# Kernel optimization log

Measured on AMD Instinct MI355X. Metric: run time of the kernel, lower is better.

Reference implementation:

```python
import jax, jax.numpy as jnp
import numpy as np
import math

B, S, D = 4, 4096, 1024
H, DH = 16, 64          # n_heads x head_dim = d_model
INTER = 4096            # intermediate_size
CAP = int(S * 0.25)     # MoD capacity = capacity_factor * seq_len = 1024


def rmsnorm(x, w, eps=1e-6):
    return x * jax.lax.rsqrt(jnp.mean(x * x, axis=-1, keepdims=True) + eps) * w


def setup_inputs() -> dict:
    key = jax.random.key(0)
    ks = jax.random.split(key, 12)
    s = 1.0 / math.sqrt(D)
    return {
        "hidden_states": jax.random.normal(ks[0], (B, S, D), jnp.float32),
        "ssm_norm_w": jnp.ones((D,), jnp.float32),
        "ssm_a": jax.random.normal(ks[1], (D,), jnp.float32),
        "ssm_gain": jax.random.normal(ks[2], (D,), jnp.float32) * 0.1,
        "router_w": jax.random.normal(ks[3], (D,), jnp.float32) * s,
        "attn_norm_w": jnp.ones((D,), jnp.float32),
        "wq": jax.random.normal(ks[4], (D, D), jnp.float32) * s,
        "wk": jax.random.normal(ks[5], (D, D), jnp.float32) * s,
        "wv": jax.random.normal(ks[6], (D, D), jnp.float32) * s,
        "wo": jax.random.normal(ks[7], (D, D), jnp.float32) * s,
        "ffn_norm_w": jnp.ones((D,), jnp.float32),
        "w1": jax.random.normal(ks[8], (D, INTER), jnp.float32) * s,
        "w2": jax.random.normal(ks[9], (INTER, D), jnp.float32) / math.sqrt(INTER),
    }


def reference(hidden_states, ssm_norm_w, ssm_a, ssm_gain, router_w, attn_norm_w,
              wq, wk, wv, wo, ffn_norm_w, w1, w2):
    # --- SSM layer (pre-norm diagonal linear recurrence + residual) ---
    xb = rmsnorm(hidden_states, ssm_norm_w)
    decay = jax.nn.sigmoid(ssm_a)  # [D] per-channel state decay

    def step(hprev, xt):  # xt: [B, D]
        hnew = decay * hprev + (1.0 - decay) * xt
        return hnew, hnew

    _, ys = jax.lax.scan(step, jnp.zeros((B, D), jnp.float32), jnp.swapaxes(xb, 0, 1))
    h = hidden_states + jnp.swapaxes(ys, 0, 1) * ssm_gain  # [B, S, D]

    # --- MoD router: pick top-CAP tokens per sequence ---
    scores = jnp.einsum('bsd,d->bs', h, router_w)            # [B, S]
    _, idx = jax.lax.top_k(scores, CAP)                      # [B, C]
    idx = jnp.sort(idx, axis=-1)                             # keep causal order
    weights = jax.nn.sigmoid(jnp.take_along_axis(scores, idx, axis=1))  # [B, C]
    aux_loss = jnp.mean(jax.nn.sigmoid(scores))              # router load aux

    # --- gather selected tokens -> attention ---
    sel = jnp.take_along_axis(h, idx[:, :, None], axis=1)    # [B, C, D]
    xn = rmsnorm(sel, attn_norm_w)
    q = (xn @ wq).reshape(B, CAP, H, DH)
    k = (xn @ wk).reshape(B, CAP, H, DH)
    v = (xn @ wv).reshape(B, CAP, H, DH)
    att = jnp.einsum('bqhd,bkhd->bhqk', q, k) / math.sqrt(DH)
    causal = jnp.tril(jnp.ones((CAP, CAP), bool))
    att = jnp.where(causal, att, jnp.float32(-1e30))
    p = jax.nn.softmax(att, axis=-1)
    o = jnp.einsum('bhqk,bkhd->bqhd', p, v).reshape(B, CAP, D)
    attn_out = o @ wo                                        # [B, C, D]

    # --- weighted scatter_add back onto the residual stream ---
    b_idx = jnp.arange(B)[:, None]
    h = h.at[b_idx, idx].add(attn_out * weights[:, :, None])

    # --- dense FFN residual (non-MoE layer) ---
    xf = rmsnorm(h, ffn_norm_w)
    h = h + jax.nn.silu(xf @ w1) @ w2
    return h, aux_loss
```

## Files before the change

kernel.cpp:

```cpp
#include <hip/hip_runtime.h>

typedef unsigned short u16;
typedef unsigned int   u32;
typedef __attribute__((ext_vector_type(4))) float f32x4;
typedef __attribute__((ext_vector_type(8))) __bf16 bf16x8;
typedef __attribute__((ext_vector_type(8))) unsigned short u16x8;

#define DEV __device__ __forceinline__

DEV u16 f2bf(float f){
  u32 u = __builtin_bit_cast(u32, f);
  u32 r = (u + 0x7fffu + ((u >> 16) & 1u)) >> 16;
  return (u16)r;
}

DEV f32x4 mfma16(bf16x8 a, bf16x8 b, f32x4 c){
  return __builtin_amdgcn_mfma_f32_16x16x32_bf16(a, b, c, 0, 0, 0);
}

DEV void gload16(const void* g, void* l){
  __builtin_amdgcn_global_load_lds((const __attribute__((address_space(1))) u32*)g,
                                   (__attribute__((address_space(3))) u32*)l, 16, 0, 0);
}

DEV int swz16(int r, int g){ return r*64 + 8*(g ^ (r&7) ^ ((r>>3)&7)); }
DEV int swze (int r, int e){ return r*64 + (e&7) + 8*(((e>>3) ^ (r&7) ^ ((r>>3)&7))); }

__global__ __launch_bounds__(256) void transpose_cast(const float* __restrict__ src,
                                                      u16* __restrict__ dst, int R, int C){
  __shared__ float tile[32][33];
  int r  = threadIdx.x >> 3;
  int c4 = (threadIdx.x & 7) * 4;
  int r0 = blockIdx.x * 32, c0 = blockIdx.y * 32;
  float4 v = *(const float4*)&src[(size_t)(r0 + r) * C + c0 + c4];
  tile[r][c4+0] = v.x; tile[r][c4+1] = v.y; tile[r][c4+2] = v.z; tile[r][c4+3] = v.w;
  __syncthreads();
  ushort4 o;
  o.x = f2bf(tile[c4+0][r]);
  o.y = f2bf(tile[c4+1][r]);
  o.z = f2bf(tile[c4+2][r]);
  o.w = f2bf(tile[c4+3][r]);
  *(ushort4*)&dst[(size_t)(c0 + r) * R + r0 + c4] = o;
}

__global__ __launch_bounds__(256) void rms_inv_k(const float* __restrict__ x, float* __restrict__ inv){
  int row  = blockIdx.x * 4 + (threadIdx.x >> 6);
  int lane = threadIdx.x & 63;
  const float* p = x + (size_t)row * 1024;
  float ss = 0.f;
  #pragma unroll
  for (int j = 0; j < 4; ++j){
    float4 v = *(const float4*)&p[lane*4 + j*256];
    ss += v.x*v.x + v.y*v.y + v.z*v.z + v.w*v.w;
  }
  #pragma unroll
  for (int o = 1; o < 64; o <<= 1) ss += __shfl_xor(ss, o);
  if (lane == 0) inv[row] = 1.f / sqrtf(ss * (1.f/1024.f) + 1e-6f);
}

__global__ __launch_bounds__(1024) void ssm_a_k(const float* __restrict__ hid, const float* __restrict__ invr,
    const float* __restrict__ nw, const float* __restrict__ av, float* __restrict__ Fc){
  int c = blockIdx.x & 63, b = blockIdx.x >> 6;
  int d = threadIdx.x;
  float w   = nw[d];
  float dec = 1.f/(1.f + expf(-av[d]));
  float od  = 1.f - dec;
  const float* hp = hid + ((size_t)b*4096 + c*64)*1024 + d;
  const float* ip = invr + b*4096 + c*64;
  float hs = 0.f;
  for (int i = 0; i < 64; ++i)
    hs = dec*hs + od*(hp[(size_t)i*1024] * ip[i] * w);
  Fc[((size_t)b*64 + c)*1024 + d] = hs;
}
__global__ __launch_bounds__(1024) void ssm_b_k(const float* __restrict__ Fc, float* __restrict__ Init,
                                                const float* __restrict__ av){
  int b  = blockIdx.x >> 6;
  int dg = blockIdx.x & 63;
  int dl = threadIdx.x >> 6;
  int c  = threadIdx.x & 63;
  int d  = dg*16 + dl;
  float dec = 1.f/(1.f + expf(-av[d]));
  float a = powf(dec, 64.f);
  float x = Fc[((size_t)(b*64 + c))*1024 + d];
  float coef = a;
  #pragma unroll
  for (int s = 1; s < 64; s <<= 1){
    float prev = __shfl_up(x, s, 64);
    if (c >= s) x += coef * prev;
    coef *= coef;
  }
  float ex = __shfl_up(x, 1, 64);
  Init[((size_t)(b*64 + c))*1024 + d] = (c > 0) ? ex : 0.f;
}
__global__ __launch_bounds__(1024) void ssm_c_k(const float* __restrict__ hid, const float* __restrict__ invr,
    const float* __restrict__ nw, const float* __restrict__ av, const float* __restrict__ gn,
    const float* __restrict__ Init, float* __restrict__ hout){
  int c = blockIdx.x & 63, b = blockIdx.x >> 6;
  int d = threadIdx.x;
  float w   = nw[d];
  float g   = gn[d];
  float dec = 1.f/(1.f + expf(-av[d]));
  float od  = 1.f - dec;
  size_t rowoff = ((size_t)b*4096 + c*64)*1024 + d;
  const float* hp = hid + rowoff;
  float* op = hout + rowoff;
  const float* ip = invr + b*4096 + c*64;
  float hs = Init[((size_t)b*64 + c)*1024 + d];
  for (int i = 0; i < 64; ++i){
    float hv = hp[(size_t)i*1024];
    hs = dec*hs + od*(hv * ip[i] * w);
    op[(size_t)i*1024] = hv + hs*g;
  }
}

__global__ __launch_bounds__(256) void score_k(const float* __restrict__ h, const float* __restrict__ rw,
                                               float* __restrict__ sc){
  int row  = blockIdx.x * 4 + (threadIdx.x >> 6);
  int lane = threadIdx.x & 63;
  const float* p = h + (size_t)row * 1024;
  float s = 0.f;
  #pragma unroll
  for (int j = 0; j < 4; ++j){
    float4 v = *(const float4*)&p[lane*4 + j*256];
    float4 w = *(const float4*)&rw[lane*4 + j*256];
    s += v.x*w.x + v.y*w.y + v.z*w.z + v.w*w.w;
  }
  #pragma unroll
  for (int o = 1; o < 64; o <<= 1) s += __shfl_xor(s, o);
  if (lane == 0) sc[row] = s;
}

__global__ __launch_bounds__(256) void aux_k(const float* __restrict__ sc, float* __restrict__ out){
  __shared__ float red[256];
  int tid = threadIdx.x;
  float s = 0.f;
  for (int i = tid; i < 16384; i += 256) s += 1.f/(1.f + expf(-sc[i]));
  red[tid] = s; __syncthreads();
  for (int o = 128; o > 0; o >>= 1){ if (tid < o) red[tid] += red[tid+o]; __syncthreads(); }
  if (tid == 0) out[0] = red[0] * (1.f/16384.f);
}

__global__ __launch_bounds__(1024) void topk_k(const float* __restrict__ sc, int* __restrict__ idx,
                                               float* __restrict__ wsel){
  __shared__ float sv[4096];
  __shared__ int   si[4096];
  int b = blockIdx.x, tid = threadIdx.x;
  for (int i = tid; i < 4096; i += 1024){ sv[i] = sc[b*4096 + i]; si[i] = i; }
  __syncthreads();
  for (int k = 2; k <= 4096; k <<= 1)
    for (int j = k >> 1; j > 0; j >>= 1){
      for (int i = tid; i < 4096; i += 1024){
        int p = i ^ j;
        if (p > i){
          float vi = sv[i], vp = sv[p];
          int ii = si[i], ip = si[p];
          bool before = (vi > vp) || (vi == vp && ii < ip);
          bool desc = ((i & k) == 0);
          if (desc ? !before : before){ sv[i]=vp; sv[p]=vi; si[i]=ip; si[p]=ii; }
        }
      }
      __syncthreads();
    }
  for (int k = 2; k <= 1024; k <<= 1)
    for (int j = k >> 1; j > 0; j >>= 1){
      int i = tid, p = i ^ j;
      if (p > i){
        int a = si[i], c = si[p];
        bool asc = ((i & k) == 0);
        if (asc ? (a > c) : (a < c)){ si[i] = c; si[p] = a; }
      }
      __syncthreads();
    }
  int t = si[tid];
  idx[b*1024 + tid]  = t;
  wsel[b*1024 + tid] = 1.f/(1.f + expf(-sc[b*4096 + t]));
}

__global__ __launch_bounds__(256) void rownorm_bf16_k(const float* __restrict__ src, const float* __restrict__ w,
    u16* __restrict__ dst, const int* __restrict__ gidx, int base){
  int row  = blockIdx.x * 4 + (threadIdx.x >> 6);
  int lane = threadIdx.x & 63;
  size_t srow;
  if (gidx){ int b = row >> 10; srow = (size_t)b*4096 + gidx[row]; }
  else srow = (size_t)(base + row);
  const float* p = src + srow*1024;
  float4 v[4]; float ss = 0.f;
  #pragma unroll
  for (int j = 0; j < 4; ++j){
    v[j] = *(const float4*)&p[lane*4 + j*256];
    ss += v[j].x*v[j].x + v[j].y*v[j].y + v[j].z*v[j].z + v[j].w*v[j].w;
  }
  #pragma unroll
  for (int o = 1; o < 64; o <<= 1) ss += __shfl_xor(ss, o);
  float inv = 1.f / sqrtf(ss * (1.f/1024.f) + 1e-6f);
  #pragma unroll
  for (int j = 0; j < 4; ++j){
    float4 wv = *(const float4*)&w[lane*4 + j*256];
    ushort4 o4;
    o4.x = f2bf(v[j].x*inv*wv.x);
    o4.y = f2bf(v[j].y*inv*wv.y);
    o4.z = f2bf(v[j].z*inv*wv.z);
    o4.w = f2bf(v[j].w*inv*wv.w);
    *(ushort4*)&dst[(size_t)row*1024 + lane*4 + j*256] = o4;
  }
}

template<int BM, int BN, int EPI>
__global__ __launch_bounds__(256) void gemmk(const u16* __restrict__ A, const u16* __restrict__ BT,
    u16* __restrict__ Cb, float* __restrict__ Cf, int M, int N, int K,
    const int* __restrict__ gidx, const float* __restrict__ wsel){
  constexpr int WROWS = BM / 2;
  constexpr int WCOLS = BN / 2;
  constexpr int MI = WROWS / 16;
  constexpr int NI = WCOLS / 16;
  constexpr int AR = BM / 32;
  constexpr int BR = BN / 32;
  __shared__ u16 As[2][BM*64];
  __shared__ u16 Bs[2][BN*64];

  int tid = threadIdx.x, wave = tid >> 6, lane = tid & 63;
  int lr = lane & 15, lg = lane >> 4;
  int wm = wave >> 1, wn = wave & 1;

  int lin = blockIdx.x + gridDim.x * blockIdx.y;
  int nwg = gridDim.x * gridDim.y;
  int q8 = nwg >> 3, r8 = nwg & 7;
  int xc = lin & 7, of = lin >> 3;
  int sw = (xc < r8 ? xc*(q8+1) : r8*(q8+1) + (xc-r8)*q8) + of;
  int bm = sw % gridDim.x, bn = sw / gridDim.x;

  f32x4 zero4 = {0.f,0.f,0.f,0.f};
  f32x4 acc[MI][NI];
  #pragma unroll
  for (int mi = 0; mi < MI; ++mi)
    #pragma unroll
    for (int ni = 0; ni < NI; ++ni) acc[mi][ni] = zero4;

  int srow = tid >> 3;
  int sgrp = (lane & 7) ^ (srow & 7);
  const size_t Kb = (size_t)K * 2;
  const char* aptr[AR];
  const char* bptr[BR];
  #pragma unroll
  for (int rr = 0; rr < AR; ++rr)
    aptr[rr] = (const char*)A + (size_t)(bm*BM + rr*32 + srow) * Kb + sgrp*16;
  #pragma unroll
  for (int rr = 0; rr < BR; ++rr)
    bptr[rr] = (const char*)BT + (size_t)(bn*BN + rr*32 + srow) * Kb + sgrp*16;

  int nkt = K >> 6;

#define STAGE(T, BUF) do { \
    size_t koff = (size_t)(T) << 7; \
    _Pragma("unroll") \
    for (int rr = 0; rr < AR; ++rr) gload16(aptr[rr] + koff, &As[BUF][(rr*32 + wave*8)*64]); \
    _Pragma("unroll") \
    for (int rr = 0; rr < BR; ++rr) gload16(bptr[rr] + koff, &Bs[BUF][(rr*32 + wave*8)*64]); \
  } while(0)

  STAGE(0, 0);
  __syncthreads();

  for (int kt = 0; kt < nkt; ++kt){
    int bi = kt & 1;
    if (kt + 1 < nkt) STAGE(kt+1, bi^1);
    __builtin_amdgcn_sched_barrier(0);

    bf16x8 bfrag[NI][2];
    #pragma unroll
    for (int ni = 0; ni < NI; ++ni)
      #pragma unroll
      for (int ks = 0; ks < 2; ++ks){
        int row = wn*WCOLS + ni*16 + lr;
        int gl = (ks*4 + lg) ^ (row & 7);
        bfrag[ni][ks] = *(const bf16x8*)&Bs[bi][row*64 + gl*8];
      }
    bf16x8 afrag[MI][2];
    #pragma unroll
    for (int mi = 0; mi < MI; ++mi)
      #pragma unroll
      for (int ks = 0; ks < 2; ++ks){
        int row = wm*WROWS + mi*16 + lr;
        int gl = (ks*4 + lg) ^ (row & 7);
        afrag[mi][ks] = *(const bf16x8*)&As[bi][row*64 + gl*8];
      }
    #pragma unroll
    for (int mi = 0; mi < MI; ++mi)
      #pragma unroll
      for (int ni = 0; ni < NI; ++ni){
        f32x4 a = acc[mi][ni];
        a = mfma16(afrag[mi][0], bfrag[ni][0], a);
        a = mfma16(afrag[mi][1], bfrag[ni][1], a);
        acc[mi][ni] = a;
      }
    __syncthreads();
  }
#undef STAGE

  #pragma unroll
  for (int mi = 0; mi < MI; ++mi){
    int rb = bm*BM + wm*WROWS + mi*16 + lg*4;
    #pragma unroll
    for (int ni = 0; ni < NI; ++ni){
      int col = bn*BN + wn*WCOLS + ni*16 + lr;
      f32x4 v = acc[mi][ni];
      if constexpr (EPI == 0){
        #pragma unroll
        for (int t = 0; t < 4; ++t) Cb[(size_t)(rb+t)*N + col] = f2bf(v[t]);
      } else if constexpr (EPI == 1){
        #pragma unroll
        for (int t = 0; t < 4; ++t){ float x = v[t]; Cb[(size_t)(rb+t)*N + col] = f2bf(x / (1.f + expf(-x))); }
      } else if constexpr (EPI == 2){
        #pragma unroll
        for (int t = 0; t < 4; ++t) Cf[(size_t)(rb+t)*N + col] += v[t];
      } else {
        #pragma unroll
        for (int t = 0; t < 4; ++t){
          int rr = rb + t;
          int bb = rr >> 10;
          float* hr = Cf + ((size_t)bb*4096 + gidx[rr])*1024;
          hr[col] += v[t] * wsel[rr];
        }
      }
    }
  }
}

__global__ __launch_bounds__(256) void attn_k(const u16* __restrict__ qkv, u16* __restrict__ obuf){
  __shared__ u16 Ks[2][4096];
  __shared__ u16 Vt[2][4096];
  __shared__ u16 Pl[8][1024];
  int blk = blockIdx.x;
  int panel = blk & 63, qp = blk >> 6;
  int b = panel >> 4, hh = panel & 15;
  int qa = qp, qb = 15 - qp;
  int tid = threadIdx.x;
  int wave = tid >> 6, lane = tid & 63;
  int lr = lane & 15, lg = lane >> 4;

  bf16x8 qf[2][2];
  int qset[2] = {qa, qb};
  #pragma unroll
  for (int s = 0; s < 2; ++s){
    const u16* qrow = qkv + (size_t)(b*1024 + qset[s]*64 + wave*16 + lr)*3072 + hh*64;
    qf[s][0] = *(const bf16x8*)(qrow + lg*8);
    qf[s][1] = *(const bf16x8*)(qrow + 32 + lg*8);
  }

  f32x4 zero4 = {0.f,0.f,0.f,0.f};
  f32x4 oacc[2][4];
  float m[2][4], sden[2][4];
  #pragma unroll
  for (int s = 0; s < 2; ++s){
    #pragma unroll
    for (int d = 0; d < 4; ++d) oacc[s][d] = zero4;
    #pragma unroll
    for (int t = 0; t < 4; ++t){ m[s][t] = -INFINITY; sden[s][t] = 0.f; }
  }

  int key0 = tid >> 3,         ce0 = (tid & 7) * 8;
  int key1 = (tid + 256) >> 3, ce1 = ((tid + 256) & 7) * 8;
  u16x8 kreg0, kreg1, vreg0, vreg1;
  const u16* kvbase = qkv + (size_t)(b*1024)*3072 + 1024 + hh*64;
  {
    const u16* g0 = kvbase + (size_t)key0*3072 + ce0;
    const u16* g1 = kvbase + (size_t)key1*3072 + ce1;
    kreg0 = *(const u16x8*)g0;  vreg0 = *(const u16x8*)(g0 + 1024);
    kreg1 = *(const u16x8*)g1;  vreg1 = *(const u16x8*)(g1 + 1024);
  }
  *(u16x8*)&Ks[0][swz16(key0, ce0 >> 3)] = kreg0;
  *(u16x8*)&Ks[0][swz16(key1, ce1 >> 3)] = kreg1;
  #pragma unroll
  for (int j = 0; j < 8; ++j) Vt[0][swze(ce0 + j, key0)] = vreg0[j];
  #pragma unroll
  for (int j = 0; j < 8; ++j) Vt[0][swze(ce1 + j, key1)] = vreg1[j];
  __syncthreads();

  for (int kt = 0; kt <= qb; ++kt){
    int bi = kt & 1;
    if (kt < qb){
      const u16* g0 = kvbase + (size_t)((kt+1)*64 + key0)*3072 + ce0;
      const u16* g1 = kvbase + (size_t)((kt+1)*64 + key1)*3072 + ce1;
      kreg0 = *(const u16x8*)g0;  vreg0 = *(const u16x8*)(g0 + 1024);
      kreg1 = *(const u16x8*)g1;  vreg1 = *(const u16x8*)(g1 + 1024);
    }
    bool act0 = (kt <= qa);

    float sv[2][4][4];
    #pragma unroll
    for (int kb = 0; kb < 4; ++kb){
      bf16x8 k0f = *(const bf16x8*)&Ks[bi][swz16(kb*16 + lr, lg)];
      bf16x8 k1f = *(const bf16x8*)&Ks[bi][swz16(kb*16 + lr, 4 + lg)];
      if (act0){
        f32x4 sa = zero4;
        sa = mfma16(qf[0][0], k0f, sa);
        sa = mfma16(qf[0][1], k1f, sa);
        #pragma unroll
        for (int t = 0; t < 4; ++t) sv[0][kb][t] = sa[t]*0.125f;
      }
      f32x4 sb = zero4;
      sb = mfma16(qf[1][0], k0f, sb);
      sb = mfma16(qf[1][1], k1f, sb);
      #pragma unroll
      for (int t = 0; t < 4; ++t) sv[1][kb][t] = sb[t]*0.125f;
    }
    #pragma unroll
    for (int s = 0; s < 2; ++s){
      if (s == 0 && !act0) continue;
      if (kt == qset[s]){
        #pragma unroll
        for (int kb = 0; kb < 4; ++kb){
          int keyg = kb*16 + lr;
          #pragma unroll
          for (int t = 0; t < 4; ++t){
            int qg = wave*16 + lg*4 + t;
            if (keyg > qg) sv[s][kb][t] = -1e30f;
          }
        }
      }
      float mn[4], scale[4];
      #pragma unroll
      for (int t = 0; t < 4; ++t){
        float tm = fmaxf(fmaxf(sv[s][0][t], sv[s][1][t]), fmaxf(sv[s][2][t], sv[s][3][t]));
        #pragma unroll
        for (int o = 1; o < 16; o <<= 1) tm = fmaxf(tm, __shfl_xor(tm, o));
        mn[t] = fmaxf(m[s][t], tm);
        scale[t] = expf(m[s][t] - mn[t]);
        m[s][t] = mn[t];
      }
      u16* Pw = &Pl[wave*2 + s][0];
      float ps[4] = {0.f,0.f,0.f,0.f};
      #pragma unroll
      for (int kb = 0; kb < 4; ++kb)
        #pragma unroll
        for (int t = 0; t < 4; ++t){
          float p = expf(sv[s][kb][t] - mn[t]);
          ps[t] += p;
          Pw[swze(lg*4 + t, kb*16 + lr)] = f2bf(p);
        }
      #pragma unroll
      for (int t = 0; t < 4; ++t){
        #pragma unroll
        for (int o = 1; o < 16; o <<= 1) ps[t] += __shfl_xor(ps[t], o);
        sden[s][t] = sden[s][t]*scale[t] + ps[t];
      }
      #pragma unroll
      for (int d = 0; d < 4; ++d){
        f32x4 v = oacc[s][d];
        #pragma unroll
        for (int t = 0; t < 4; ++t) v[t] *= scale[t];
        oacc[s][d] = v;
      }
    }
    bf16x8 pa[2][2];
    if (act0){
      pa[0][0] = *(const bf16x8*)&Pl[wave*2][swz16(lr, lg)];
      pa[0][1] = *(const bf16x8*)&Pl[wave*2][swz16(lr, 4 + lg)];
    }
    pa[1][0] = *(const bf16x8*)&Pl[wave*2+1][swz16(lr, lg)];
    pa[1][1] = *(const bf16x8*)&Pl[wave*2+1][swz16(lr, 4 + lg)];
    #pragma unroll
    for (int d = 0; d < 4; ++d){
      bf16x8 v0 = *(const bf16x8*)&Vt[bi][swz16(d*16 + lr, lg)];
      bf16x8 v1 = *(const bf16x8*)&Vt[bi][swz16(d*16 + lr, 4 + lg)];
      if (act0){
        oacc[0][d] = mfma16(pa[0][0], v0, oacc[0][d]);
        oacc[0][d] = mfma16(pa[0][1], v1, oacc[0][d]);
      }
      oacc[1][d] = mfma16(pa[1][0], v0, oacc[1][d]);
      oacc[1][d] = mfma16(pa[1][1], v1, oacc[1][d]);
    }
    if (kt < qb){
      *(u16x8*)&Ks[bi^1][swz16(key0, ce0 >> 3)] = kreg0;
      *(u16x8*)&Ks[bi^1][swz16(key1, ce1 >> 3)] = kreg1;
      #pragma unroll
      for (int j = 0; j < 8; ++j) Vt[bi^1][swze(ce0 + j, key0)] = vreg0[j];
      #pragma unroll
      for (int j = 0; j < 8; ++j) Vt[bi^1][swze(ce1 + j, key1)] = vreg1[j];
      __syncthreads();
    }
  }

  #pragma unroll
  for (int s = 0; s < 2; ++s)
    #pragma unroll
    for (int d = 0; d < 4; ++d)
      #pragma unroll
      for (int t = 0; t < 4; ++t){
        int qrel = qset[s]*64 + wave*16 + lg*4 + t;
        float val = oacc[s][d][t] / sden[s][t];
        obuf[(size_t)(b*1024 + qrel)*1024 + hh*64 + d*16 + lr] = f2bf(val);
      }
}

extern "C" void kernel_launch(void* const* d_in, const int* in_sizes, int n_in,
                              void* d_out, int out_size, void* d_ws, size_t ws_size,
                              hipStream_t stream) {
  const float* hid    = (const float*)d_in[0];
  const float* nssm   = (const float*)d_in[1];
  const float* ssma   = (const float*)d_in[2];
  const float* ssmg   = (const float*)d_in[3];
  const float* routw  = (const float*)d_in[4];
  const float* nattn  = (const float*)d_in[5];
  const float* wq     = (const float*)d_in[6];
  const float* wk     = (const float*)d_in[7];
  const float* wv     = (const float*)d_in[8];
  const float* wo     = (const float*)d_in[9];
  const float* nffn   = (const float*)d_in[10];
  const float* w1     = (const float*)d_in[11];
  const float* w2     = (const float*)d_in[12];

  float* hbuf = (float*)d_out;
  char* wsb = (char*)d_ws;
  u16*   wqkvT  = (u16*)(wsb + 0);
  u16*   woT    = (u16*)(wsb + 6291456);
  u16*   w1T    = (u16*)(wsb + 8388608);
  u16*   w2T    = (u16*)(wsb + 16777216);
  float* invr   = (float*)(wsb + 25165824);
  float* scores = (float*)(wsb + 25231360);
  float* Fc     = (float*)(wsb + 25296896);
  float* Init   = (float*)(wsb + 26345472);
  int*   idxb   = (int*)(wsb + 27394048);
  float* wselb  = (float*)(wsb + 27410432);
  u16*   xn     = (u16*)(wsb + 27426816);
  u16*   qkv    = (u16*)(wsb + 35815424);
  u16*   obuf   = (u16*)(wsb + 60981248);
  u16*   xf     = (u16*)(wsb + 27394048);
  u16*   act    = (u16*)(wsb + 35782656);

  transpose_cast<<<dim3(32,32),  256, 0, stream>>>(wq, wqkvT,              1024, 1024);
  transpose_cast<<<dim3(32,32),  256, 0, stream>>>(wk, wqkvT + 1048576,    1024, 1024);
  transpose_cast<<<dim3(32,32),  256, 0, stream>>>(wv, wqkvT + 2097152,    1024, 1024);
  transpose_cast<<<dim3(32,32),  256, 0, stream>>>(wo, woT,                1024, 1024);
  transpose_cast<<<dim3(32,128), 256, 0, stream>>>(w1, w1T,                1024, 4096);
  transpose_cast<<<dim3(128,32), 256, 0, stream>>>(w2, w2T,                4096, 1024);

  rms_inv_k<<<4096, 256, 0, stream>>>(hid, invr);
  ssm_a_k<<<256, 1024, 0, stream>>>(hid, invr, nssm, ssma, Fc);
  ssm_b_k<<<256, 1024, 0, stream>>>(Fc, Init, ssma);
  ssm_c_k<<<256, 1024, 0, stream>>>(hid, invr, nssm, ssma, ssmg, Init, hbuf);

  score_k<<<4096, 256, 0, stream>>>(hbuf, routw, scores);
  aux_k<<<1, 256, 0, stream>>>(scores, hbuf + 16777216);
  topk_k<<<4, 1024, 0, stream>>>(scores, idxb, wselb);

  rownorm_bf16_k<<<1024, 256, 0, stream>>>(hbuf, nattn, xn, idxb, 0);
  gemmk<128,128,0><<<dim3(32,24), 256, 0, stream>>>(xn, wqkvT, qkv, nullptr, 4096, 3072, 1024, nullptr, nullptr);
  attn_k<<<512, 256, 0, stream>>>(qkv, obuf);
  gemmk<64,128,3><<<dim3(64,8), 256, 0, stream>>>(obuf, woT, nullptr, hbuf, 4096, 1024, 1024, idxb, wselb);

  for (int ch = 0; ch < 4; ++ch){
    int m0 = ch * 4096;
    rownorm_bf16_k<<<1024, 256, 0, stream>>>(hbuf, nffn, xf, nullptr, m0);
    gemmk<128,128,1><<<dim3(32,32), 256, 0, stream>>>(xf, w1T, act, nullptr, 4096, 4096, 1024, nullptr, nullptr);
    gemmk<64,128,2><<<dim3(64,8), 256, 0, stream>>>(act, w2T, nullptr, hbuf + (size_t)m0*1024, 4096, 1024, 4096, nullptr, nullptr);
  }
  (void)in_sizes; (void)n_in; (void)out_size; (void)ws_size;
}
```

Baseline: 787.3 us.

## Replace bitonic top-k with radix select and shrink GEMM K-tile to 32

Three separate changes. The top-k kernel's full bitonic sort plus index re-sort is replaced by a 4-pass 8-bit radix select on order-preserving float keys, followed by a prefix-scan compaction that writes the selected indices already in ascending order. The GEMM K-tile is halved from 64 to 32, which halves LDS use per block, uses one MFMA per fragment pair per step, and switches to a 4-way XOR swizzle. The wo and w2 GEMMs now use 128x64 tiles instead of 64x128. The smaller K-tile doubles the number of loop iterations and barriers, which may reduce MFMA utilisation in the large FFN GEMMs.

```diff
diff --git a/kernel.cpp b/kernel.cpp
--- a/kernel.cpp
+++ b/kernel.cpp
@@ -142,38 +142,74 @@
 
 __global__ __launch_bounds__(1024) void topk_k(const float* __restrict__ sc, int* __restrict__ idx,
                                                float* __restrict__ wsel){
-  __shared__ float sv[4096];
-  __shared__ int   si[4096];
+  __shared__ u32 keys[4096];
+  __shared__ int hist[256];
+  __shared__ int wsum[16];
+  __shared__ int sel_info[2];
   int b = blockIdx.x, tid = threadIdx.x;
-  for (int i = tid; i < 4096; i += 1024){ sv[i] = sc[b*4096 + i]; si[i] = i; }
+  for (int i = tid; i < 4096; i += 1024){
+    u32 u = __builtin_bit_cast(u32, sc[b*4096 + i]);
+    keys[i] = u ^ ((u32)((int)u >> 31) | 0x80000000u);
+  }
+  int k = 1024;
+  u32 prefix = 0, mask = 0;
+  for (int level = 3; level >= 0; --level){
+    __syncthreads();
+    if (tid < 256) hist[tid] = 0;
+    __syncthreads();
+    int sh = level*8;
+    for (int i = tid; i < 4096; i += 1024){
+      u32 kk = keys[i];
+      if ((kk & mask) == prefix) atomicAdd(&hist[(kk >> sh) & 255], 1);
+    }
+    __syncthreads();
+    if (tid == 0){
+      int cum = 0, bb = 255;
+      for (; bb > 0; --bb){
+        if (cum + hist[bb] >= k) break;
+        cum += hist[bb];
+      }
+      sel_info[0] = bb; sel_info[1] = k - cum;
+    }
+    __syncthreads();
+    prefix |= ((u32)sel_info[0]) << sh;
+    mask |= 0xffu << sh;
+    k = sel_info[1];
+  }
+  u32 T = prefix;
+  int base = tid*4;
+  u32 k4[4]; int cgt = 0, ceq = 0;
+  #pragma unroll
+  for (int j = 0; j < 4; ++j){
+    k4[j] = keys[base+j];
+    cgt += (k4[j] > T); ceq += (k4[j] == T);
+  }
+  int val = cgt | (ceq << 13);
+  int incl = val;
+  #pragma unroll
+  for (int o = 1; o < 64; o <<= 1){ int t = __shfl_up(incl, o, 64); if ((tid&63) >= o) incl += t; }
+  int wid = tid >> 6;
+  if ((tid&63) == 63) wsum[wid] = incl;
   __syncthreads();
-  for (int k = 2; k <= 4096; k <<= 1)
-    for (int j = k >> 1; j > 0; j >>= 1){
-      for (int i = tid; i < 4096; i += 1024){
-        int p = i ^ j;
-        if (p > i){
-          float vi = sv[i], vp = sv[p];
-          int ii = si[i], ip = si[p];
-          bool before = (vi > vp) || (vi == vp && ii < ip);
-          bool desc = ((i & k) == 0);
-          if (desc ? !before : before){ sv[i]=vp; sv[p]=vi; si[i]=ip; si[p]=ii; }
-        }
-      }
-      __syncthreads();
-    }
-  for (int k = 2; k <= 1024; k <<= 1)
-    for (int j = k >> 1; j > 0; j >>= 1){
-      int i = tid, p = i ^ j;
-      if (p > i){
-        int a = si[i], c = si[p];
-        bool asc = ((i & k) == 0);
-        if (asc ? (a > c) : (a < c)){ si[i] = c; si[p] = a; }
-      }
-      __syncthreads();
-    }
-  int t = si[tid];
-  idx[b*1024 + tid]  = t;
-  wsel[b*1024 + tid] = 1.f/(1.f + expf(-sc[b*4096 + t]));
+  if (tid < 16){
+    int v = wsum[tid];
+    #pragma unroll
+    for (int o = 1; o < 16; o <<= 1){ int t = __shfl_up(v, o, 64); if (tid >= o) v += t; }
+    wsum[tid] = v;
+  }
+  __syncthreads();
+  int excl = incl - val + (wid > 0 ? wsum[wid-1] : 0);
+  int g = excl & 0x1fff, e = excl >> 13;
+  #pragma unroll
+  for (int j = 0; j < 4; ++j){
+    bool isgt = (k4[j] > T), iseq = (k4[j] == T);
+    if (isgt || (iseq && e < k)){
+      int pos = g + (e < k ? e : k);
+      idx[b*1024 + pos]  = base + j;
+      wsel[b*1024 + pos] = 1.f/(1.f + expf(-sc[b*4096 + base + j]));
+    }
+    g += isgt; e += iseq;
+  }
 }
 
 __global__ __launch_bounds__(256) void rownorm_bf16_k(const float* __restrict__ src, const float* __restrict__ w,
@@ -213,10 +249,10 @@
   constexpr int WCOLS = BN / 2;
   constexpr int MI = WROWS / 16;
   constexpr int NI = WCOLS / 16;
-  constexpr int AR = BM / 32;
-  constexpr int BR = BN / 32;
-  __shared__ u16 As[2][BM*64];
-  __shared__ u16 Bs[2][BN*64];
+  constexpr int AR = BM / 64;
+  constexpr int BR = BN / 64;
+  __shared__ u16 As[2][BM*32];
+  __shared__ u16 Bs[2][BN*32];
 
   int tid = threadIdx.x, wave = tid >> 6, lane = tid & 63;
   int lr = lane & 15, lg = lane >> 4;
@@ -236,26 +272,26 @@
     #pragma unroll
     for (int ni = 0; ni < NI; ++ni) acc[mi][ni] = zero4;
 
-  int srow = tid >> 3;
-  int sgrp = (lane & 7) ^ (srow & 7);
+  int srow = wave*16 + (lane >> 2);
+  int sgrp = (lane & 3) ^ ((lane >> 2) & 3);
   const size_t Kb = (size_t)K * 2;
   const char* aptr[AR];
   const char* bptr[BR];
   #pragma unroll
   for (int rr = 0; rr < AR; ++rr)
-    aptr[rr] = (const char*)A + (size_t)(bm*BM + rr*32 + srow) * Kb + sgrp*16;
+    aptr[rr] = (const char*)A + (size_t)(bm*BM + rr*64 + srow) * Kb + sgrp*16;
   #pragma unroll
   for (int rr = 0; rr < BR; ++rr)
-    bptr[rr] = (const char*)BT + (size_t)(bn*BN + rr*32 + srow) * Kb + sgrp*16;
-
-  int nkt = K >> 6;
+    bptr[rr] = (const char*)BT + (size_t)(bn*BN + rr*64 + srow) * Kb + sgrp*16;
+
+  int nkt = K >> 5;
 
 #define STAGE(T, BUF) do { \
-    size_t koff = (size_t)(T) << 7; \
+    size_t koff = (size_t)(T) << 6; \
     _Pragma("unroll") \
-    for (int rr = 0; rr < AR; ++rr) gload16(aptr[rr] + koff, &As[BUF][(rr*32 + wave*8)*64]); \
+    for (int rr = 0; rr < AR; ++rr) gload16(aptr[rr] + koff, (char*)&As[BUF][0] + rr*4096 + wave*1024); \
     _Pragma("unroll") \
-    for (int rr = 0; rr < BR; ++rr) gload16(bptr[rr] + koff, &Bs[BUF][(rr*32 + wave*8)*64]); \
+    for (int rr = 0; rr < BR; ++rr) gload16(bptr[rr] + koff, (char*)&Bs[BUF][0] + rr*4096 + wave*1024); \
   } while(0)
 
   STAGE(0, 0);
@@ -266,33 +302,23 @@
     if (kt + 1 < nkt) STAGE(kt+1, bi^1);
     __builtin_amdgcn_sched_barrier(0);
 
-    bf16x8 bfrag[NI][2];
-    #pragma unroll
-    for (int ni = 0; ni < NI; ++ni)
-      #pragma unroll
-      for (int ks = 0; ks < 2; ++ks){
-        int row = wn*WCOLS + ni*16 + lr;
-        int gl = (ks*4 + lg) ^ (row & 7);
-        bfrag[ni][ks] = *(const bf16x8*)&Bs[bi][row*64 + gl*8];
-      }
-    bf16x8 afrag[MI][2];
+    bf16x8 bfrag[NI];
+    #pragma unroll
+    for (int ni = 0; ni < NI; ++ni){
+      int row = wn*WCOLS + ni*16 + lr;
+      bfrag[ni] = *(const bf16x8*)&Bs[bi][row*32 + ((lg ^ (row & 3))*8)];
+    }
+    bf16x8 afrag[MI];
+    #pragma unroll
+    for (int mi = 0; mi < MI; ++mi){
+      int row = wm*WROWS + mi*16 + lr;
+      afrag[mi] = *(const bf16x8*)&As[bi][row*32 + ((lg ^ (row & 3))*8)];
+    }
     #pragma unroll
     for (int mi = 0; mi < MI; ++mi)
       #pragma unroll
-      for (int ks = 0; ks < 2; ++ks){
-        int row = wm*WROWS + mi*16 + lr;
-        int gl = (ks*4 + lg) ^ (row & 7);
-        afrag[mi][ks] = *(const bf16x8*)&As[bi][row*64 + gl*8];
-      }
-    #pragma unroll
-    for (int mi = 0; mi < MI; ++mi)
-      #pragma unroll
-      for (int ni = 0; ni < NI; ++ni){
-        f32x4 a = acc[mi][ni];
-        a = mfma16(afrag[mi][0], bfrag[ni][0], a);
-        a = mfma16(afrag[mi][1], bfrag[ni][1], a);
-        acc[mi][ni] = a;
-      }
+      for (int ni = 0; ni < NI; ++ni)
+        acc[mi][ni] = mfma16(afrag[mi], bfrag[ni], acc[mi][ni]);
     __syncthreads();
   }
 #undef STAGE
@@ -547,13 +573,13 @@
   rownorm_bf16_k<<<1024, 256, 0, stream>>>(hbuf, nattn, xn, idxb, 0);
   gemmk<128,128,0><<<dim3(32,24), 256, 0, stream>>>(xn, wqkvT, qkv, nullptr, 4096, 3072, 1024, nullptr, nullptr);
   attn_k<<<512, 256, 0, stream>>>(qkv, obuf);
-  gemmk<64,128,3><<<dim3(64,8), 256, 0, stream>>>(obuf, woT, nullptr, hbuf, 4096, 1024, 1024, idxb, wselb);
+  gemmk<128,64,3><<<dim3(32,16), 256, 0, stream>>>(obuf, woT, nullptr, hbuf, 4096, 1024, 1024, idxb, wselb);
 
   for (int ch = 0; ch < 4; ++ch){
     int m0 = ch * 4096;
     rownorm_bf16_k<<<1024, 256, 0, stream>>>(hbuf, nffn, xf, nullptr, m0);
     gemmk<128,128,1><<<dim3(32,32), 256, 0, stream>>>(xf, w1T, act, nullptr, 4096, 4096, 1024, nullptr, nullptr);
-    gemmk<64,128,2><<<dim3(64,8), 256, 0, stream>>>(act, w2T, nullptr, hbuf + (size_t)m0*1024, 4096, 1024, 4096, nullptr, nullptr);
+    gemmk<128,64,2><<<dim3(32,16), 256, 0, stream>>>(act, w2T, nullptr, hbuf + (size_t)m0*1024, 4096, 1024, 4096, nullptr, nullptr);
   }
   (void)in_sizes; (void)n_in; (void)out_size; (void)ws_size;
 }
```

Measured after the change: 787.6 us. About the same (+0.0%).
